# Performance work log

Measured on AMD Instinct MI355X. Metric: run time of the kernel, lower is better.

The kernel has to match this reference:

```python
import jax, jax.numpy as jnp
import numpy as np

B, T, D, H = 4096, 48, 64, 128
IMPUTE_WEIGHT = 0.3


def setup_inputs() -> dict:
    key = jax.random.key(0)
    ks = jax.random.split(key, 16)
    values = jax.random.normal(ks[0], (B, T, D), dtype=jnp.float32)
    masks = (jax.random.uniform(ks[1], (B, T, D)) < 0.7).astype(jnp.float32)
    deltas = jax.random.uniform(ks[2], (B, T, D), dtype=jnp.float32)
    s = 0.05
    return {
        "values": values, "masks": masks, "deltas": deltas,
        # TemporalDecay h (non-diag): Linear(D -> H)
        "W_td_h": jax.random.normal(ks[3], (H, D), dtype=jnp.float32) * s,
        "b_td_h": jax.random.normal(ks[4], (H,), dtype=jnp.float32) * s,
        # TemporalDecay x (diag): W is D x D but only diagonal used
        "W_td_x": jax.random.normal(ks[5], (D, D), dtype=jnp.float32) * s,
        "b_td_x": jax.random.normal(ks[6], (D,), dtype=jnp.float32) * s,
        # hist_reg: Linear(H -> D)
        "W_hist": jax.random.normal(ks[7], (D, H), dtype=jnp.float32) * s,
        "b_hist": jax.random.normal(ks[8], (D,), dtype=jnp.float32) * s,
        # feat_reg: D x D with zeroed diagonal mask
        "W_feat": jax.random.normal(ks[9], (D, D), dtype=jnp.float32) * s,
        "b_feat": jax.random.normal(ks[10], (D,), dtype=jnp.float32) * s,
        # weight_combine: Linear(2D -> D)
        "W_comb": jax.random.normal(ks[11], (D, 2 * D), dtype=jnp.float32) * s,
        "b_comb": jax.random.normal(ks[12], (D,), dtype=jnp.float32) * s,
        # LSTMCell(2D -> H), torch gate order i,f,g,o
        "W_ih": jax.random.normal(ks[13], (4 * H, 2 * D), dtype=jnp.float32) * s,
        "W_hh": jax.random.normal(ks[14], (4 * H, H), dtype=jnp.float32) * s,
        "b_ih": jnp.zeros((4 * H,), dtype=jnp.float32),
        "b_hh": jnp.zeros((4 * H,), dtype=jnp.float32),
    }


def reference(values, masks, deltas, W_td_h, b_td_h, W_td_x, b_td_x,
              W_hist, b_hist, W_feat, b_feat, W_comb, b_comb,
              W_ih, W_hh, b_ih, b_hh):
    Bn, Tn, Dn = values.shape
    Hn = W_hh.shape[1]
    w_td_x_diag = jnp.diagonal(W_td_x)                      # diag mask -> elementwise
    W_feat_m = W_feat * (1.0 - jnp.eye(Dn, dtype=W_feat.dtype))  # zero diagonal

    def step(carry, xs):
        h, c, x_loss = carry
        x, m, d = xs                                        # each [B, D]
        gamma_h = jnp.exp(-jax.nn.relu(d @ W_td_h.T + b_td_h))   # [B, H]
        gamma_x = jnp.exp(-jax.nn.relu(d * w_td_x_diag + b_td_x))  # [B, D]
        h = h * gamma_h
        x_h = h @ W_hist.T + b_hist
        denom = jnp.sum(m) + 1e-5
        x_loss = x_loss + jnp.sum(jnp.abs(x - x_h) * m) / denom
        x_c = m * x + (1.0 - m) * x_h
        z_h = x_c @ W_feat_m.T + b_feat
        x_loss = x_loss + jnp.sum(jnp.abs(x - z_h) * m) / denom
        alpha = jnp.concatenate([gamma_x, m], axis=1) @ W_comb.T + b_comb
        c_h = alpha * z_h + (1.0 - alpha) * x_h
        x_loss = x_loss + jnp.sum(jnp.abs(x - c_h) * m) / denom
        c_c = m * x + (1.0 - m) * c_h
        inp = jnp.concatenate([c_c, m], axis=1)             # [B, 2D]
        gates = inp @ W_ih.T + b_ih + h @ W_hh.T + b_hh     # [B, 4H]
        i_g, f_g, g_g, o_g = jnp.split(gates, 4, axis=1)
        c = jax.nn.sigmoid(f_g) * c + jax.nn.sigmoid(i_g) * jnp.tanh(g_g)
        h = jax.nn.sigmoid(o_g) * jnp.tanh(c)
        return (h, c, x_loss), c_c

    h0 = jnp.zeros((Bn, Hn), dtype=values.dtype)
    c0 = jnp.zeros((Bn, Hn), dtype=values.dtype)
    xs = (jnp.swapaxes(values, 0, 1), jnp.swapaxes(masks, 0, 1), jnp.swapaxes(deltas, 0, 1))
    (_, _, x_loss), imps = jax.lax.scan(step, (h0, c0, jnp.float32(0.0)), xs)
    imputations = jnp.swapaxes(imps, 0, 1)                  # [B, T, D]
    loss = x_loss * IMPUTE_WEIGHT
    return loss, imputations
```

## Files before the change

kernel.cpp:

```cpp
#include <hip/hip_runtime.h>
#include <cmath>

#define Bb 4096
#define Tt 48
#define Dd 64
#define Hh 128
#define NB 16
#define NTHR 512

typedef unsigned short ushort_t;
typedef __attribute__((ext_vector_type(8))) short short8;
typedef __attribute__((ext_vector_type(4))) float floatx4;

#define WS_DEN   0
#define WS_LOSS  48
#define WS_FRAGS 64
#define FR_F 0
#define FR_A 256
#define FR_B 272
#define FR_C 288
#define FR_E 296
#define N_FRAGS 312

__device__ __forceinline__ ushort_t f2bf(float x) {
  unsigned int u = __float_as_uint(x);
  u += 0x7fffu + ((u >> 16) & 1u);
  return (ushort_t)(u >> 16);
}
__device__ __forceinline__ float sigmoidf_(float x) { return 1.0f / (1.0f + __expf(-x)); }
__device__ __forceinline__ float tanhf_(float x) { return 2.0f / (1.0f + __expf(-2.0f * x)) - 1.0f; }

__global__ void prep_kernel(const float* __restrict__ W_td_h, const float* __restrict__ W_hist,
                            const float* __restrict__ W_feat, const float* __restrict__ W_comb,
                            const float* __restrict__ W_ih, const float* __restrict__ W_hh,
                            float* __restrict__ ws) {
  int f = blockIdx.x;
  int tid = threadIdx.x;
  if (f == 0 && tid < 64) ws[tid] = 0.0f;
  ushort_t* fb = (ushort_t*)(ws + WS_FRAGS);
  #pragma unroll
  for (int u = 0; u < 2; u++) {
    int e = tid * 2 + u;
    int l = e >> 3, j = e & 7;
    int n16 = l & 15;
    int kq = ((l >> 4) << 3) + j;
    float v;
    if (f < 256) {
      int w = f >> 5, g = (f >> 3) & 3, ks = f & 7;
      int n = g * 128 + w * 16 + n16;
      int k = ks * 32 + kq;
      v = (k < 128) ? W_ih[n * 128 + k] : W_hh[n * 128 + (k - 128)];
    } else if (f < 272) {
      int ff = f - 256, w = ff >> 1, ks = ff & 1;
      int n = w * 16 + n16;
      v = W_td_h[n * 64 + ks * 32 + kq];
    } else if (f < 288) {
      int ff = f - 272, w = ff >> 2, ks = ff & 3;
      int n = w * 16 + n16;
      v = W_hist[n * 128 + ks * 32 + kq];
    } else if (f < 296) {
      int ff = f - 288, w = ff >> 1, ks = ff & 1;
      int n = w * 16 + n16;
      int k = ks * 32 + kq;
      v = (n == k) ? 0.0f : W_feat[n * 64 + k];
    } else {
      int ff = f - 296, w = ff >> 2, ks = ff & 3;
      int n = w * 16 + n16;
      v = W_comb[n * 128 + ks * 32 + kq];
    }
    fb[f * 512 + e] = f2bf(v);
  }
}

__global__ void denom_kernel(const float* __restrict__ masks, float* __restrict__ ws) {
  int t = blockIdx.x >> 4;
  int chunk = blockIdx.x & 15;
  int base = chunk * 256;
  int tid = threadIdx.x;
  int j = tid & 63;
  int brow = tid >> 6;
  float s = 0.0f;
  for (int i = 0; i < 64; i++) {
    int b = base + i * 4 + brow;
    s += masks[((size_t)b * Tt + t) * Dd + j];
  }
  for (int off = 32; off > 0; off >>= 1) s += __shfl_down(s, off, 64);
  __shared__ float red[4];
  if ((tid & 63) == 0) red[tid >> 6] = s;
  __syncthreads();
  if (tid == 0) atomicAdd(&ws[WS_DEN + t], red[0] + red[1] + red[2] + red[3]);
}

__global__ __launch_bounds__(NTHR, 2)
void main_kernel(const float* __restrict__ values, const float* __restrict__ masks,
                 const float* __restrict__ deltas, const float* __restrict__ W_td_x,
                 const float* __restrict__ b_td_h, const float* __restrict__ b_td_x,
                 const float* __restrict__ b_hist, const float* __restrict__ b_feat,
                 const float* __restrict__ b_comb,
                 const float* __restrict__ b_ih, const float* __restrict__ b_hh,
                 float* ws, float* __restrict__ out) {
  __shared__ __align__(16) ushort_t act[16 * 264];
  __shared__ __align__(16) ushort_t dbuf[16 * 72];
  __shared__ __align__(16) ushort_t gxbuf[16 * 72];
  __shared__ __align__(16) ushort_t xcbuf[16 * 72];
  __shared__ __align__(16) float xmbuf[16 * 132];
  __shared__ __align__(16) float xhbuf[16 * 68];
  __shared__ float red[8];

  int tid = threadIdx.x;
  int w = tid >> 6;
  int lane = tid & 63;
  int l15 = lane & 15;
  int quad = lane >> 4;
  int b0 = blockIdx.x * NB;
  const ushort_t* fb = (const ushort_t*)(ws + WS_FRAGS);

  short8 wF[32];
  #pragma unroll
  for (int g = 0; g < 4; g++)
    #pragma unroll
    for (int ks = 0; ks < 8; ks++)
      wF[g * 8 + ks] = *(const short8*)(fb + (size_t)(FR_F + w * 32 + g * 8 + ks) * 512 + lane * 8);
  short8 wA[2];
  #pragma unroll
  for (int ks = 0; ks < 2; ks++)
    wA[ks] = *(const short8*)(fb + (size_t)(FR_A + w * 2 + ks) * 512 + lane * 8);
  short8 wBE[4];
  short8 wC[2];
  if (w < 4) {
    #pragma unroll
    for (int ks = 0; ks < 4; ks++)
      wBE[ks] = *(const short8*)(fb + (size_t)(FR_B + w * 4 + ks) * 512 + lane * 8);
  } else {
    #pragma unroll
    for (int ks = 0; ks < 4; ks++)
      wBE[ks] = *(const short8*)(fb + (size_t)(FR_E + (w - 4) * 4 + ks) * 512 + lane * 8);
    #pragma unroll
    for (int ks = 0; ks < 2; ks++)
      wC[ks] = *(const short8*)(fb + (size_t)(FR_C + (w - 4) * 2 + ks) * 512 + lane * 8);
  }

  int colh = w * 16 + l15;
  float biasF0 = b_ih[colh]       + b_hh[colh];
  float biasF1 = b_ih[128 + colh] + b_hh[128 + colh];
  float biasF2 = b_ih[256 + colh] + b_hh[256 + colh];
  float biasF3 = b_ih[384 + colh] + b_hh[384 + colh];
  float biasA  = b_td_h[colh];
  int colD = (w & 3) * 16 + l15;
  float biasBE = (w < 4) ? b_hist[colD] : b_comb[colD];
  float biasC  = b_feat[colD];

  int e0 = tid * 2;
  int lb = e0 >> 6, li = e0 & 63;
  size_t gbase = ((size_t)(b0 + lb) * Tt) * Dd + li;
  float diag0 = W_td_x[li * 64 + li], diag1 = W_td_x[(li + 1) * 64 + (li + 1)];
  float btx0 = b_td_x[li], btx1 = b_td_x[li + 1];

  int ha[4];
  float* impp[4];
  #pragma unroll
  for (int r = 0; r < 4; r++) {
    int m = quad * 4 + r;
    ha[r] = m * 264 + 128 + colh;
    impp[r] = out + 1 + (size_t)(b0 + m) * Tt * Dd + colD;
  }

  float h_reg[4] = {0.f, 0.f, 0.f, 0.f};
  float c_reg[4] = {0.f, 0.f, 0.f, 0.f};
  float loss_acc = 0.0f;

  float2 px = *(const float2*)(values + gbase);
  float2 pm = *(const float2*)(masks + gbase);
  float2 pd = *(const float2*)(deltas + gbase);

  for (int t = 0; t < Tt; t++) {
    __syncthreads();
    *(float4*)(&xmbuf[lb * 132 + 2 * li]) = make_float4(px.x, pm.x, px.y, pm.y);
    *(unsigned int*)(&act[lb * 264 + 64 + li]) =
        (unsigned int)f2bf(pm.x) | ((unsigned int)f2bf(pm.y) << 16);
    *(unsigned int*)(&dbuf[lb * 72 + li]) =
        (unsigned int)f2bf(pd.x) | ((unsigned int)f2bf(pd.y) << 16);
    float g0 = __expf(-fmaxf(pd.x * diag0 + btx0, 0.0f));
    float g1 = __expf(-fmaxf(pd.y * diag1 + btx1, 0.0f));
    *(unsigned int*)(&gxbuf[lb * 72 + li]) =
        (unsigned int)f2bf(g0) | ((unsigned int)f2bf(g1) << 16);
    float invden = 1.0f / (ws[WS_DEN + t] + 1e-5f);
    floatx4 a0 = {biasF0, biasF0, biasF0, biasF0};
    floatx4 a1 = {biasF1, biasF1, biasF1, biasF1};
    floatx4 a2 = {biasF2, biasF2, biasF2, biasF2};
    floatx4 a3 = {biasF3, biasF3, biasF3, biasF3};
    {
      int tn = (t + 1 < Tt) ? (t + 1) : t;
      size_t g = gbase + (size_t)tn * Dd;
      px = *(const float2*)(values + g);
      pm = *(const float2*)(masks + g);
      pd = *(const float2*)(deltas + g);
    }
    __syncthreads();

    short8 mf0 = *(const short8*)(&act[l15 * 264 + 64 + quad * 8]);
    short8 mf1 = *(const short8*)(&act[l15 * 264 + 96 + quad * 8]);
    {
      short8 df0 = *(const short8*)(&dbuf[l15 * 72 + quad * 8]);
      short8 df1 = *(const short8*)(&dbuf[l15 * 72 + 32 + quad * 8]);
      floatx4 accA = {biasA, biasA, biasA, biasA};
      accA = __builtin_amdgcn_mfma_f32_16x16x32_bf16(df0, wA[0], accA, 0, 0, 0);
      accA = __builtin_amdgcn_mfma_f32_16x16x32_bf16(df1, wA[1], accA, 0, 0, 0);
      a0 = __builtin_amdgcn_mfma_f32_16x16x32_bf16(mf0, wF[2],  a0, 0, 0, 0);
      a0 = __builtin_amdgcn_mfma_f32_16x16x32_bf16(mf1, wF[3],  a0, 0, 0, 0);
      a1 = __builtin_amdgcn_mfma_f32_16x16x32_bf16(mf0, wF[10], a1, 0, 0, 0);
      a1 = __builtin_amdgcn_mfma_f32_16x16x32_bf16(mf1, wF[11], a1, 0, 0, 0);
      a2 = __builtin_amdgcn_mfma_f32_16x16x32_bf16(mf0, wF[18], a2, 0, 0, 0);
      a2 = __builtin_amdgcn_mfma_f32_16x16x32_bf16(mf1, wF[19], a2, 0, 0, 0);
      a3 = __builtin_amdgcn_mfma_f32_16x16x32_bf16(mf0, wF[26], a3, 0, 0, 0);
      a3 = __builtin_amdgcn_mfma_f32_16x16x32_bf16(mf1, wF[27], a3, 0, 0, 0);
      #pragma unroll
      for (int r = 0; r < 4; r++) {
        h_reg[r] *= __expf(-fmaxf(accA[r], 0.0f));
        act[ha[r]] = f2bf(h_reg[r]);
      }
    }
    __syncthreads();

    floatx4 accP = {biasBE, biasBE, biasBE, biasBE};
    {
      short8 hf0 = *(const short8*)(&act[l15 * 264 + 128 + quad * 8]);
      short8 hf1 = *(const short8*)(&act[l15 * 264 + 160 + quad * 8]);
      short8 hf2 = *(const short8*)(&act[l15 * 264 + 192 + quad * 8]);
      short8 hf3 = *(const short8*)(&act[l15 * 264 + 224 + quad * 8]);
      if (w < 4) {
        accP = __builtin_amdgcn_mfma_f32_16x16x32_bf16(hf0, wBE[0], accP, 0, 0, 0);
        accP = __builtin_amdgcn_mfma_f32_16x16x32_bf16(hf1, wBE[1], accP, 0, 0, 0);
        accP = __builtin_amdgcn_mfma_f32_16x16x32_bf16(hf2, wBE[2], accP, 0, 0, 0);
        accP = __builtin_amdgcn_mfma_f32_16x16x32_bf16(hf3, wBE[3], accP, 0, 0, 0);
      } else {
        short8 gx0 = *(const short8*)(&gxbuf[l15 * 72 + quad * 8]);
        short8 gx1 = *(const short8*)(&gxbuf[l15 * 72 + 32 + quad * 8]);
        accP = __builtin_amdgcn_mfma_f32_16x16x32_bf16(gx0, wBE[0], accP, 0, 0, 0);
        accP = __builtin_amdgcn_mfma_f32_16x16x32_bf16(gx1, wBE[1], accP, 0, 0, 0);
        accP = __builtin_amdgcn_mfma_f32_16x16x32_bf16(mf0, wBE[2], accP, 0, 0, 0);
        accP = __builtin_amdgcn_mfma_f32_16x16x32_bf16(mf1, wBE[3], accP, 0, 0, 0);
      }
      a0 = __builtin_amdgcn_mfma_f32_16x16x32_bf16(hf0, wF[4],  a0, 0, 0, 0);
      a0 = __builtin_amdgcn_mfma_f32_16x16x32_bf16(hf1, wF[5],  a0, 0, 0, 0);
      a0 = __builtin_amdgcn_mfma_f32_16x16x32_bf16(hf2, wF[6],  a0, 0, 0, 0);
      a0 = __builtin_amdgcn_mfma_f32_16x16x32_bf16(hf3, wF[7],  a0, 0, 0, 0);
      a1 = __builtin_amdgcn_mfma_f32_16x16x32_bf16(hf0, wF[12], a1, 0, 0, 0);
      a1 = __builtin_amdgcn_mfma_f32_16x16x32_bf16(hf1, wF[13], a1, 0, 0, 0);
      a1 = __builtin_amdgcn_mfma_f32_16x16x32_bf16(hf2, wF[14], a1, 0, 0, 0);
      a1 = __builtin_amdgcn_mfma_f32_16x16x32_bf16(hf3, wF[15], a1, 0, 0, 0);
      a2 = __builtin_amdgcn_mfma_f32_16x16x32_bf16(hf0, wF[20], a2, 0, 0, 0);
      a2 = __builtin_amdgcn_mfma_f32_16x16x32_bf16(hf1, wF[21], a2, 0, 0, 0);
      a2 = __builtin_amdgcn_mfma_f32_16x16x32_bf16(hf2, wF[22], a2, 0, 0, 0);
      a2 = __builtin_amdgcn_mfma_f32_16x16x32_bf16(hf3, wF[23], a2, 0, 0, 0);
      a3 = __builtin_amdgcn_mfma_f32_16x16x32_bf16(hf0, wF[28], a3, 0, 0, 0);
      a3 = __builtin_amdgcn_mfma_f32_16x16x32_bf16(hf1, wF[29], a3, 0, 0, 0);
      a3 = __builtin_amdgcn_mfma_f32_16x16x32_bf16(hf2, wF[30], a3, 0, 0, 0);
      a3 = __builtin_amdgcn_mfma_f32_16x16x32_bf16(hf3, wF[31], a3, 0, 0, 0);
      if (w < 4) {
        #pragma unroll
        for (int r = 0; r < 4; r++) {
          int m = quad * 4 + r;
          float2 xm = *(const float2*)(&xmbuf[m * 132 + 2 * colD]);
          float xh = accP[r];
          loss_acc += fabsf(xm.x - xh) * xm.y * invden;
          xhbuf[m * 68 + colD] = xh;
          xcbuf[m * 72 + colD] = f2bf(xm.y * xm.x + (1.0f - xm.y) * xh);
        }
      }
    }
    __syncthreads();

    if (w >= 4) {
      short8 xc0 = *(const short8*)(&xcbuf[l15 * 72 + quad * 8]);
      short8 xc1 = *(const short8*)(&xcbuf[l15 * 72 + 32 + quad * 8]);
      floatx4 accC = {biasC, biasC, biasC, biasC};
      accC = __builtin_amdgcn_mfma_f32_16x16x32_bf16(xc0, wC[0], accC, 0, 0, 0);
      accC = __builtin_amdgcn_mfma_f32_16x16x32_bf16(xc1, wC[1], accC, 0, 0, 0);
      #pragma unroll
      for (int r = 0; r < 4; r++) {
        int m = quad * 4 + r;
        float2 xm = *(const float2*)(&xmbuf[m * 132 + 2 * colD]);
        float xh = xhbuf[m * 68 + colD];
        float zh = accC[r];
        float al = accP[r];
        loss_acc += fabsf(xm.x - zh) * xm.y * invden;
        float ch = al * zh + (1.0f - al) * xh;
        loss_acc += fabsf(xm.x - ch) * xm.y * invden;
        float cc = xm.y * xm.x + (1.0f - xm.y) * ch;
        *impp[r] = cc;
        impp[r] += Dd;
        act[m * 264 + colD] = f2bf(cc);
      }
    } else {
      #pragma unroll
      for (int r = 0; r < 4; r++) impp[r] += Dd;
    }
    __syncthreads();

    {
      short8 cf0 = *(const short8*)(&act[l15 * 264 + quad * 8]);
      short8 cf1 = *(const short8*)(&act[l15 * 264 + 32 + quad * 8]);
      a0 = __builtin_amdgcn_mfma_f32_16x16x32_bf16(cf0, wF[0],  a0, 0, 0, 0);
      a0 = __builtin_amdgcn_mfma_f32_16x16x32_bf16(cf1, wF[1],  a0, 0, 0, 0);
      a1 = __builtin_amdgcn_mfma_f32_16x16x32_bf16(cf0, wF[8],  a1, 0, 0, 0);
      a1 = __builtin_amdgcn_mfma_f32_16x16x32_bf16(cf1, wF[9],  a1, 0, 0, 0);
      a2 = __builtin_amdgcn_mfma_f32_16x16x32_bf16(cf0, wF[16], a2, 0, 0, 0);
      a2 = __builtin_amdgcn_mfma_f32_16x16x32_bf16(cf1, wF[17], a2, 0, 0, 0);
      a3 = __builtin_amdgcn_mfma_f32_16x16x32_bf16(cf0, wF[24], a3, 0, 0, 0);
      a3 = __builtin_amdgcn_mfma_f32_16x16x32_bf16(cf1, wF[25], a3, 0, 0, 0);
      #pragma unroll
      for (int r = 0; r < 4; r++) {
        float ig = sigmoidf_(a0[r]);
        float fg = sigmoidf_(a1[r]);
        float gg = tanhf_(a2[r]);
        float og = sigmoidf_(a3[r]);
        c_reg[r] = fg * c_reg[r] + ig * gg;
        h_reg[r] = og * tanhf_(c_reg[r]);
      }
    }
  }

  float s = loss_acc;
  for (int off = 32; off > 0; off >>= 1) s += __shfl_down(s, off, 64);
  if (lane == 0) red[w] = s;
  __syncthreads();
  if (tid == 0) {
    float tot = 0.0f;
    #pragma unroll
    for (int i = 0; i < 8; i++) tot += red[i];
    atomicAdd(&ws[WS_LOSS], tot);
  }
}

__global__ void final_kernel(const float* __restrict__ ws, float* __restrict__ out) {
  if (threadIdx.x == 0 && blockIdx.x == 0) out[0] = 0.3f * ws[WS_LOSS];
}

extern "C" void kernel_launch(void* const* d_in, const int* in_sizes, int n_in,
                              void* d_out, int out_size, void* d_ws, size_t ws_size,
                              hipStream_t stream) {
  const float* values = (const float*)d_in[0];
  const float* masks  = (const float*)d_in[1];
  const float* deltas = (const float*)d_in[2];
  const float* W_td_h = (const float*)d_in[3];
  const float* b_td_h = (const float*)d_in[4];
  const float* W_td_x = (const float*)d_in[5];
  const float* b_td_x = (const float*)d_in[6];
  const float* W_hist = (const float*)d_in[7];
  const float* b_hist = (const float*)d_in[8];
  const float* W_feat = (const float*)d_in[9];
  const float* b_feat = (const float*)d_in[10];
  const float* W_comb = (const float*)d_in[11];
  const float* b_comb = (const float*)d_in[12];
  const float* W_ih   = (const float*)d_in[13];
  const float* W_hh   = (const float*)d_in[14];
  const float* b_ih   = (const float*)d_in[15];
  const float* b_hh   = (const float*)d_in[16];
  float* out = (float*)d_out;
  float* ws  = (float*)d_ws;

  prep_kernel<<<dim3(N_FRAGS), dim3(256), 0, stream>>>(W_td_h, W_hist, W_feat, W_comb,
                                                       W_ih, W_hh, ws);
  denom_kernel<<<dim3(48 * 16), dim3(256), 0, stream>>>(masks, ws);
  main_kernel<<<dim3(Bb / NB), dim3(NTHR), 0, stream>>>(values, masks, deltas, W_td_x,
                                                        b_td_h, b_td_x, b_hist, b_feat,
                                                        b_comb, b_ih, b_hh, ws, out);
  final_kernel<<<dim3(1), dim3(64), 0, stream>>>(ws, out);
}
```

Baseline: 375.2 us.

## Split LSTM gate work across 16 waves and defer cell-update MFMAs

Doubles the block to 1024 threads so that each group of eight waves owns two of the four LSTM gates, and the workers for the hist, feat and comb regressions are spread over separate waves. Gate activations are exchanged through a new shared buffer. The c_c-dependent gate MFMAs and the cell update are deferred to the start of the next timestep, which removes one block barrier per step. The aim is more MFMA and VALU parallelism per CU and a shorter per-step dependency chain, at the cost of more shared memory, extra LDS traffic and tighter register limits under launch_bounds(1024,4).

```diff
diff --git a/kernel.cpp b/kernel.cpp
--- a/kernel.cpp
+++ b/kernel.cpp
@@ -6,7 +6,7 @@
 #define Dd 64
 #define Hh 128
 #define NB 16
-#define NTHR 512
+#define NTHR 1024
 
 typedef unsigned short ushort_t;
 typedef __attribute__((ext_vector_type(8))) short short8;
@@ -46,26 +46,26 @@
     int kq = ((l >> 4) << 3) + j;
     float v;
     if (f < 256) {
-      int w = f >> 5, g = (f >> 3) & 3, ks = f & 7;
-      int n = g * 128 + w * 16 + n16;
+      int cg = f >> 5, g = (f >> 3) & 3, ks = f & 7;
+      int n = g * 128 + cg * 16 + n16;
       int k = ks * 32 + kq;
       v = (k < 128) ? W_ih[n * 128 + k] : W_hh[n * 128 + (k - 128)];
     } else if (f < 272) {
-      int ff = f - 256, w = ff >> 1, ks = ff & 1;
-      int n = w * 16 + n16;
+      int ff = f - 256, cg = ff >> 1, ks = ff & 1;
+      int n = cg * 16 + n16;
       v = W_td_h[n * 64 + ks * 32 + kq];
     } else if (f < 288) {
-      int ff = f - 272, w = ff >> 2, ks = ff & 3;
-      int n = w * 16 + n16;
+      int ff = f - 272, cd = ff >> 2, ks = ff & 3;
+      int n = cd * 16 + n16;
       v = W_hist[n * 128 + ks * 32 + kq];
     } else if (f < 296) {
-      int ff = f - 288, w = ff >> 1, ks = ff & 1;
-      int n = w * 16 + n16;
+      int ff = f - 288, cd = ff >> 1, ks = ff & 1;
+      int n = cd * 16 + n16;
       int k = ks * 32 + kq;
       v = (n == k) ? 0.0f : W_feat[n * 64 + k];
     } else {
-      int ff = f - 296, w = ff >> 2, ks = ff & 3;
-      int n = w * 16 + n16;
+      int ff = f - 296, cd = ff >> 2, ks = ff & 3;
+      int n = cd * 16 + n16;
       v = W_comb[n * 128 + ks * 32 + kq];
     }
     fb[f * 512 + e] = f2bf(v);
@@ -91,7 +91,7 @@
   if (tid == 0) atomicAdd(&ws[WS_DEN + t], red[0] + red[1] + red[2] + red[3]);
 }
 
-__global__ __launch_bounds__(NTHR, 2)
+__global__ __launch_bounds__(NTHR, 4)
 void main_kernel(const float* __restrict__ values, const float* __restrict__ masks,
                  const float* __restrict__ deltas, const float* __restrict__ W_td_x,
                  const float* __restrict__ b_td_h, const float* __restrict__ b_td_x,
@@ -105,91 +105,108 @@
   __shared__ __align__(16) ushort_t xcbuf[16 * 72];
   __shared__ __align__(16) float xmbuf[16 * 132];
   __shared__ __align__(16) float xhbuf[16 * 68];
-  __shared__ float red[8];
+  __shared__ __align__(16) float pbuf[4096];
+  __shared__ float red[16];
 
   int tid = threadIdx.x;
   int w = tid >> 6;
   int lane = tid & 63;
   int l15 = lane & 15;
   int quad = lane >> 4;
+  int cg = w & 7;
+  bool lo = (w < 8);
   int b0 = blockIdx.x * NB;
   const ushort_t* fb = (const ushort_t*)(ws + WS_FRAGS);
 
-  short8 wF[32];
-  #pragma unroll
-  for (int g = 0; g < 4; g++)
-    #pragma unroll
-    for (int ks = 0; ks < 8; ks++)
-      wF[g * 8 + ks] = *(const short8*)(fb + (size_t)(FR_F + w * 32 + g * 8 + ks) * 512 + lane * 8);
-  short8 wA[2];
-  #pragma unroll
-  for (int ks = 0; ks < 2; ks++)
-    wA[ks] = *(const short8*)(fb + (size_t)(FR_A + w * 2 + ks) * 512 + lane * 8);
-  short8 wBE[4];
-  short8 wC[2];
-  if (w < 4) {
+  short8 wG[16];
+  {
+    int gb = lo ? 0 : 2;
+    #pragma unroll
+    for (int lg = 0; lg < 2; lg++)
+      #pragma unroll
+      for (int ks = 0; ks < 8; ks++)
+        wG[lg * 8 + ks] =
+            *(const short8*)(fb + (size_t)(FR_F + cg * 32 + (gb + lg) * 8 + ks) * 512 + lane * 8);
+  }
+  short8 wX[6];
+  if (lo) {
+    #pragma unroll
+    for (int ks = 0; ks < 2; ks++)
+      wX[ks] = *(const short8*)(fb + (size_t)(FR_A + cg * 2 + ks) * 512 + lane * 8);
+  } else if (w < 12) {
     #pragma unroll
     for (int ks = 0; ks < 4; ks++)
-      wBE[ks] = *(const short8*)(fb + (size_t)(FR_B + w * 4 + ks) * 512 + lane * 8);
+      wX[ks] = *(const short8*)(fb + (size_t)(FR_B + (w - 8) * 4 + ks) * 512 + lane * 8);
   } else {
     #pragma unroll
     for (int ks = 0; ks < 4; ks++)
-      wBE[ks] = *(const short8*)(fb + (size_t)(FR_E + (w - 4) * 4 + ks) * 512 + lane * 8);
+      wX[ks] = *(const short8*)(fb + (size_t)(FR_E + (w - 12) * 4 + ks) * 512 + lane * 8);
     #pragma unroll
     for (int ks = 0; ks < 2; ks++)
-      wC[ks] = *(const short8*)(fb + (size_t)(FR_C + (w - 4) * 2 + ks) * 512 + lane * 8);
-  }
-
-  int colh = w * 16 + l15;
-  float biasF0 = b_ih[colh]       + b_hh[colh];
-  float biasF1 = b_ih[128 + colh] + b_hh[128 + colh];
-  float biasF2 = b_ih[256 + colh] + b_hh[256 + colh];
-  float biasF3 = b_ih[384 + colh] + b_hh[384 + colh];
-  float biasA  = b_td_h[colh];
+      wX[4 + ks] = *(const short8*)(fb + (size_t)(FR_C + (w - 12) * 2 + ks) * 512 + lane * 8);
+  }
+
+  int colh = cg * 16 + l15;
+  float biasG0, biasG1;
+  if (lo) { biasG0 = b_ih[colh] + b_hh[colh];  biasG1 = b_ih[128 + colh] + b_hh[128 + colh]; }
+  else    { biasG0 = b_ih[256 + colh] + b_hh[256 + colh];  biasG1 = b_ih[384 + colh] + b_hh[384 + colh]; }
   int colD = (w & 3) * 16 + l15;
-  float biasBE = (w < 4) ? b_hist[colD] : b_comb[colD];
-  float biasC  = b_feat[colD];
+  float biasAC = lo ? b_td_h[colh] : b_feat[colD];
+  float biasBE = (w < 12) ? b_hist[colD] : b_comb[colD];
 
   int e0 = tid * 2;
   int lb = e0 >> 6, li = e0 & 63;
-  size_t gbase = ((size_t)(b0 + lb) * Tt) * Dd + li;
-  float diag0 = W_td_x[li * 64 + li], diag1 = W_td_x[(li + 1) * 64 + (li + 1)];
-  float btx0 = b_td_x[li], btx1 = b_td_x[li + 1];
-
-  int ha[4];
-  float* impp[4];
-  #pragma unroll
-  for (int r = 0; r < 4; r++) {
-    int m = quad * 4 + r;
-    ha[r] = m * 264 + 128 + colh;
-    impp[r] = out + 1 + (size_t)(b0 + m) * Tt * Dd + colD;
-  }
-
+  size_t gbase = 0;
+  float diag0 = 0, diag1 = 0, btx0 = 0, btx1 = 0;
+  float2 px, pm, pd;
+  if (lo) {
+    gbase = ((size_t)(b0 + lb) * Tt) * Dd + li;
+    diag0 = W_td_x[li * 64 + li];  diag1 = W_td_x[(li + 1) * 64 + (li + 1)];
+    btx0 = b_td_x[li];  btx1 = b_td_x[li + 1];
+    px = *(const float2*)(values + gbase);
+    pm = *(const float2*)(masks + gbase);
+    pd = *(const float2*)(deltas + gbase);
+  }
+
+  float* impt = out + 1;
+  if (w >= 12) impt = out + 1 + (size_t)(b0 + quad * 4) * (Tt * Dd) + colD;
+
+  floatx4 aG0, aG1, accP;
   float h_reg[4] = {0.f, 0.f, 0.f, 0.f};
   float c_reg[4] = {0.f, 0.f, 0.f, 0.f};
   float loss_acc = 0.0f;
 
-  float2 px = *(const float2*)(values + gbase);
-  float2 pm = *(const float2*)(masks + gbase);
-  float2 pd = *(const float2*)(deltas + gbase);
-
   for (int t = 0; t < Tt; t++) {
     __syncthreads();
-    *(float4*)(&xmbuf[lb * 132 + 2 * li]) = make_float4(px.x, pm.x, px.y, pm.y);
-    *(unsigned int*)(&act[lb * 264 + 64 + li]) =
-        (unsigned int)f2bf(pm.x) | ((unsigned int)f2bf(pm.y) << 16);
-    *(unsigned int*)(&dbuf[lb * 72 + li]) =
-        (unsigned int)f2bf(pd.x) | ((unsigned int)f2bf(pd.y) << 16);
-    float g0 = __expf(-fmaxf(pd.x * diag0 + btx0, 0.0f));
-    float g1 = __expf(-fmaxf(pd.y * diag1 + btx1, 0.0f));
-    *(unsigned int*)(&gxbuf[lb * 72 + li]) =
-        (unsigned int)f2bf(g0) | ((unsigned int)f2bf(g1) << 16);
+    if (t > 0) {
+      short8 cf0 = *(const short8*)(&act[l15 * 264 + quad * 8]);
+      short8 cf1 = *(const short8*)(&act[l15 * 264 + 32 + quad * 8]);
+      aG0 = __builtin_amdgcn_mfma_f32_16x16x32_bf16(cf0, wG[0], aG0, 0, 0, 0);
+      aG0 = __builtin_amdgcn_mfma_f32_16x16x32_bf16(cf1, wG[1], aG0, 0, 0, 0);
+      aG1 = __builtin_amdgcn_mfma_f32_16x16x32_bf16(cf0, wG[8], aG1, 0, 0, 0);
+      aG1 = __builtin_amdgcn_mfma_f32_16x16x32_bf16(cf1, wG[9], aG1, 0, 0, 0);
+      if (!lo) {
+        #pragma unroll
+        for (int r = 0; r < 4; r++) {
+          float tg = tanhf_(aG0[r]);
+          float so = sigmoidf_(aG1[r]);
+          *(float2*)(&pbuf[((r * 8 + cg) * 64 + lane) * 2]) = make_float2(tg, so);
+        }
+      }
+    }
+    if (lo) {
+      *(float4*)(&xmbuf[lb * 132 + 2 * li]) = make_float4(px.x, pm.x, px.y, pm.y);
+      *(unsigned int*)(&act[lb * 264 + 64 + li]) =
+          (unsigned int)f2bf(pm.x) | ((unsigned int)f2bf(pm.y) << 16);
+      *(unsigned int*)(&dbuf[lb * 72 + li]) =
+          (unsigned int)f2bf(pd.x) | ((unsigned int)f2bf(pd.y) << 16);
+      float g0 = __expf(-fmaxf(pd.x * diag0 + btx0, 0.0f));
+      float g1 = __expf(-fmaxf(pd.y * diag1 + btx1, 0.0f));
+      *(unsigned int*)(&gxbuf[lb * 72 + li]) =
+          (unsigned int)f2bf(g0) | ((unsigned int)f2bf(g1) << 16);
+    }
     float invden = 1.0f / (ws[WS_DEN + t] + 1e-5f);
-    floatx4 a0 = {biasF0, biasF0, biasF0, biasF0};
-    floatx4 a1 = {biasF1, biasF1, biasF1, biasF1};
-    floatx4 a2 = {biasF2, biasF2, biasF2, biasF2};
-    floatx4 a3 = {biasF3, biasF3, biasF3, biasF3};
-    {
+    if (lo) {
       int tn = (t + 1 < Tt) ? (t + 1) : t;
       size_t g = gbase + (size_t)tn * Dd;
       px = *(const float2*)(values + g);
@@ -198,71 +215,72 @@
     }
     __syncthreads();
 
-    short8 mf0 = *(const short8*)(&act[l15 * 264 + 64 + quad * 8]);
-    short8 mf1 = *(const short8*)(&act[l15 * 264 + 96 + quad * 8]);
-    {
-      short8 df0 = *(const short8*)(&dbuf[l15 * 72 + quad * 8]);
-      short8 df1 = *(const short8*)(&dbuf[l15 * 72 + 32 + quad * 8]);
-      floatx4 accA = {biasA, biasA, biasA, biasA};
-      accA = __builtin_amdgcn_mfma_f32_16x16x32_bf16(df0, wA[0], accA, 0, 0, 0);
-      accA = __builtin_amdgcn_mfma_f32_16x16x32_bf16(df1, wA[1], accA, 0, 0, 0);
-      a0 = __builtin_amdgcn_mfma_f32_16x16x32_bf16(mf0, wF[2],  a0, 0, 0, 0);
-      a0 = __builtin_amdgcn_mfma_f32_16x16x32_bf16(mf1, wF[3],  a0, 0, 0, 0);
-      a1 = __builtin_amdgcn_mfma_f32_16x16x32_bf16(mf0, wF[10], a1, 0, 0, 0);
-      a1 = __builtin_amdgcn_mfma_f32_16x16x32_bf16(mf1, wF[11], a1, 0, 0, 0);
-      a2 = __builtin_amdgcn_mfma_f32_16x16x32_bf16(mf0, wF[18], a2, 0, 0, 0);
-      a2 = __builtin_amdgcn_mfma_f32_16x16x32_bf16(mf1, wF[19], a2, 0, 0, 0);
-      a3 = __builtin_amdgcn_mfma_f32_16x16x32_bf16(mf0, wF[26], a3, 0, 0, 0);
-      a3 = __builtin_amdgcn_mfma_f32_16x16x32_bf16(mf1, wF[27], a3, 0, 0, 0);
+    if (lo && t > 0) {
       #pragma unroll
       for (int r = 0; r < 4; r++) {
-        h_reg[r] *= __expf(-fmaxf(accA[r], 0.0f));
-        act[ha[r]] = f2bf(h_reg[r]);
+        float2 p = *(const float2*)(&pbuf[((r * 8 + cg) * 64 + lane) * 2]);
+        float ig = sigmoidf_(aG0[r]);
+        float fg = sigmoidf_(aG1[r]);
+        c_reg[r] = fg * c_reg[r] + ig * p.x;
+        h_reg[r] = p.y * tanhf_(c_reg[r]);
+      }
+    }
+    aG0 = floatx4{biasG0, biasG0, biasG0, biasG0};
+    aG1 = floatx4{biasG1, biasG1, biasG1, biasG1};
+    {
+      short8 mf0 = *(const short8*)(&act[l15 * 264 + 64 + quad * 8]);
+      short8 mf1 = *(const short8*)(&act[l15 * 264 + 96 + quad * 8]);
+      aG0 = __builtin_amdgcn_mfma_f32_16x16x32_bf16(mf0, wG[2],  aG0, 0, 0, 0);
+      aG0 = __builtin_amdgcn_mfma_f32_16x16x32_bf16(mf1, wG[3],  aG0, 0, 0, 0);
+      aG1 = __builtin_amdgcn_mfma_f32_16x16x32_bf16(mf0, wG[10], aG1, 0, 0, 0);
+      aG1 = __builtin_amdgcn_mfma_f32_16x16x32_bf16(mf1, wG[11], aG1, 0, 0, 0);
+      if (lo) {
+        short8 df0 = *(const short8*)(&dbuf[l15 * 72 + quad * 8]);
+        short8 df1 = *(const short8*)(&dbuf[l15 * 72 + 32 + quad * 8]);
+        floatx4 accA = floatx4{biasAC, biasAC, biasAC, biasAC};
+        accA = __builtin_amdgcn_mfma_f32_16x16x32_bf16(df0, wX[0], accA, 0, 0, 0);
+        accA = __builtin_amdgcn_mfma_f32_16x16x32_bf16(df1, wX[1], accA, 0, 0, 0);
+        #pragma unroll
+        for (int r = 0; r < 4; r++) {
+          h_reg[r] *= __expf(-fmaxf(accA[r], 0.0f));
+          act[(quad * 4 + r) * 264 + 128 + colh] = f2bf(h_reg[r]);
+        }
+      } else if (w >= 12) {
+        short8 gx0 = *(const short8*)(&gxbuf[l15 * 72 + quad * 8]);
+        short8 gx1 = *(const short8*)(&gxbuf[l15 * 72 + 32 + quad * 8]);
+        accP = floatx4{biasBE, biasBE, biasBE, biasBE};
+        accP = __builtin_amdgcn_mfma_f32_16x16x32_bf16(gx0, wX[0], accP, 0, 0, 0);
+        accP = __builtin_amdgcn_mfma_f32_16x16x32_bf16(gx1, wX[1], accP, 0, 0, 0);
+        accP = __builtin_amdgcn_mfma_f32_16x16x32_bf16(mf0, wX[2], accP, 0, 0, 0);
+        accP = __builtin_amdgcn_mfma_f32_16x16x32_bf16(mf1, wX[3], accP, 0, 0, 0);
       }
     }
     __syncthreads();
 
-    floatx4 accP = {biasBE, biasBE, biasBE, biasBE};
     {
       short8 hf0 = *(const short8*)(&act[l15 * 264 + 128 + quad * 8]);
       short8 hf1 = *(const short8*)(&act[l15 * 264 + 160 + quad * 8]);
       short8 hf2 = *(const short8*)(&act[l15 * 264 + 192 + quad * 8]);
       short8 hf3 = *(const short8*)(&act[l15 * 264 + 224 + quad * 8]);
-      if (w < 4) {
-        accP = __builtin_amdgcn_mfma_f32_16x16x32_bf16(hf0, wBE[0], accP, 0, 0, 0);
-        accP = __builtin_amdgcn_mfma_f32_16x16x32_bf16(hf1, wBE[1], accP, 0, 0, 0);
-        accP = __builtin_amdgcn_mfma_f32_16x16x32_bf16(hf2, wBE[2], accP, 0, 0, 0);
-        accP = __builtin_amdgcn_mfma_f32_16x16x32_bf16(hf3, wBE[3], accP, 0, 0, 0);
-      } else {
-        short8 gx0 = *(const short8*)(&gxbuf[l15 * 72 + quad * 8]);
-        short8 gx1 = *(const short8*)(&gxbuf[l15 * 72 + 32 + quad * 8]);
-        accP = __builtin_amdgcn_mfma_f32_16x16x32_bf16(gx0, wBE[0], accP, 0, 0, 0);
-        accP = __builtin_amdgcn_mfma_f32_16x16x32_bf16(gx1, wBE[1], accP, 0, 0, 0);
-        accP = __builtin_amdgcn_mfma_f32_16x16x32_bf16(mf0, wBE[2], accP, 0, 0, 0);
-        accP = __builtin_amdgcn_mfma_f32_16x16x32_bf16(mf1, wBE[3], accP, 0, 0, 0);
-      }
-      a0 = __builtin_amdgcn_mfma_f32_16x16x32_bf16(hf0, wF[4],  a0, 0, 0, 0);
-      a0 = __builtin_amdgcn_mfma_f32_16x16x32_bf16(hf1, wF[5],  a0, 0, 0, 0);
-      a0 = __builtin_amdgcn_mfma_f32_16x16x32_bf16(hf2, wF[6],  a0, 0, 0, 0);
-      a0 = __builtin_amdgcn_mfma_f32_16x16x32_bf16(hf3, wF[7],  a0, 0, 0, 0);
-      a1 = __builtin_amdgcn_mfma_f32_16x16x32_bf16(hf0, wF[12], a1, 0, 0, 0);
-      a1 = __builtin_amdgcn_mfma_f32_16x16x32_bf16(hf1, wF[13], a1, 0, 0, 0);
-      a1 = __builtin_amdgcn_mfma_f32_16x16x32_bf16(hf2, wF[14], a1, 0, 0, 0);
-      a1 = __builtin_amdgcn_mfma_f32_16x16x32_bf16(hf3, wF[15], a1, 0, 0, 0);
-      a2 = __builtin_amdgcn_mfma_f32_16x16x32_bf16(hf0, wF[20], a2, 0, 0, 0);
-      a2 = __builtin_amdgcn_mfma_f32_16x16x32_bf16(hf1, wF[21], a2, 0, 0, 0);
-      a2 = __builtin_amdgcn_mfma_f32_16x16x32_bf16(hf2, wF[22], a2, 0, 0, 0);
-      a2 = __builtin_amdgcn_mfma_f32_16x16x32_bf16(hf3, wF[23], a2, 0, 0, 0);
-      a3 = __builtin_amdgcn_mfma_f32_16x16x32_bf16(hf0, wF[28], a3, 0, 0, 0);
-      a3 = __builtin_amdgcn_mfma_f32_16x16x32_bf16(hf1, wF[29], a3, 0, 0, 0);
-      a3 = __builtin_amdgcn_mfma_f32_16x16x32_bf16(hf2, wF[30], a3, 0, 0, 0);
-      a3 = __builtin_amdgcn_mfma_f32_16x16x32_bf16(hf3, wF[31], a3, 0, 0, 0);
-      if (w < 4) {
+      aG0 = __builtin_amdgcn_mfma_f32_16x16x32_bf16(hf0, wG[4],  aG0, 0, 0, 0);
+      aG0 = __builtin_amdgcn_mfma_f32_16x16x32_bf16(hf1, wG[5],  aG0, 0, 0, 0);
+      aG0 = __builtin_amdgcn_mfma_f32_16x16x32_bf16(hf2, wG[6],  aG0, 0, 0, 0);
+      aG0 = __builtin_amdgcn_mfma_f32_16x16x32_bf16(hf3, wG[7],  aG0, 0, 0, 0);
+      aG1 = __builtin_amdgcn_mfma_f32_16x16x32_bf16(hf0, wG[12], aG1, 0, 0, 0);
+      aG1 = __builtin_amdgcn_mfma_f32_16x16x32_bf16(hf1, wG[13], aG1, 0, 0, 0);
+      aG1 = __builtin_amdgcn_mfma_f32_16x16x32_bf16(hf2, wG[14], aG1, 0, 0, 0);
+      aG1 = __builtin_amdgcn_mfma_f32_16x16x32_bf16(hf3, wG[15], aG1, 0, 0, 0);
+      if (!lo && w < 12) {
+        floatx4 accB = floatx4{biasBE, biasBE, biasBE, biasBE};
+        accB = __builtin_amdgcn_mfma_f32_16x16x32_bf16(hf0, wX[0], accB, 0, 0, 0);
+        accB = __builtin_amdgcn_mfma_f32_16x16x32_bf16(hf1, wX[1], accB, 0, 0, 0);
+        accB = __builtin_amdgcn_mfma_f32_16x16x32_bf16(hf2, wX[2], accB, 0, 0, 0);
+        accB = __builtin_amdgcn_mfma_f32_16x16x32_bf16(hf3, wX[3], accB, 0, 0, 0);
         #pragma unroll
         for (int r = 0; r < 4; r++) {
           int m = quad * 4 + r;
           float2 xm = *(const float2*)(&xmbuf[m * 132 + 2 * colD]);
-          float xh = accP[r];
+          float xh = accB[r];
           loss_acc += fabsf(xm.x - xh) * xm.y * invden;
           xhbuf[m * 68 + colD] = xh;
           xcbuf[m * 72 + colD] = f2bf(xm.y * xm.x + (1.0f - xm.y) * xh);
@@ -271,53 +289,27 @@
     }
     __syncthreads();
 
-    if (w >= 4) {
+    if (w >= 12) {
       short8 xc0 = *(const short8*)(&xcbuf[l15 * 72 + quad * 8]);
       short8 xc1 = *(const short8*)(&xcbuf[l15 * 72 + 32 + quad * 8]);
-      floatx4 accC = {biasC, biasC, biasC, biasC};
-      accC = __builtin_amdgcn_mfma_f32_16x16x32_bf16(xc0, wC[0], accC, 0, 0, 0);
-      accC = __builtin_amdgcn_mfma_f32_16x16x32_bf16(xc1, wC[1], accC, 0, 0, 0);
+      floatx4 accC = floatx4{biasAC, biasAC, biasAC, biasAC};
+      accC = __builtin_amdgcn_mfma_f32_16x16x32_bf16(xc0, wX[4], accC, 0, 0, 0);
+      accC = __builtin_amdgcn_mfma_f32_16x16x32_bf16(xc1, wX[5], accC, 0, 0, 0);
       #pragma unroll
       for (int r = 0; r < 4; r++) {
         int m = quad * 4 + r;
         float2 xm = *(const float2*)(&xmbuf[m * 132 + 2 * colD]);
-        float xh = xhbuf[m * 68 + colD];
         float zh = accC[r];
         float al = accP[r];
+        float xh = xhbuf[m * 68 + colD];
         loss_acc += fabsf(xm.x - zh) * xm.y * invden;
         float ch = al * zh + (1.0f - al) * xh;
         loss_acc += fabsf(xm.x - ch) * xm.y * invden;
         float cc = xm.y * xm.x + (1.0f - xm.y) * ch;
-        *impp[r] = cc;
-        impp[r] += Dd;
+        impt[r * (Tt * Dd)] = cc;
         act[m * 264 + colD] = f2bf(cc);
       }
-    } else {
-      #pragma unroll
-      for (int r = 0; r < 4; r++) impp[r] += Dd;
-    }
-    __syncthreads();
-
-    {
-      short8 cf0 = *(const short8*)(&act[l15 * 264 + quad * 8]);
-      short8 cf1 = *(const short8*)(&act[l15 * 264 + 32 + quad * 8]);
-      a0 = __builtin_amdgcn_mfma_f32_16x16x32_bf16(cf0, wF[0],  a0, 0, 0, 0);
-      a0 = __builtin_amdgcn_mfma_f32_16x16x32_bf16(cf1, wF[1],  a0, 0, 0, 0);
-      a1 = __builtin_amdgcn_mfma_f32_16x16x32_bf16(cf0, wF[8],  a1, 0, 0, 0);
-      a1 = __builtin_amdgcn_mfma_f32_16x16x32_bf16(cf1, wF[9],  a1, 0, 0, 0);
-      a2 = __builtin_amdgcn_mfma_f32_16x16x32_bf16(cf0, wF[16], a2, 0, 0, 0);
-      a2 = __builtin_amdgcn_mfma_f32_16x16x32_bf16(cf1, wF[17], a2, 0, 0, 0);
-      a3 = __builtin_amdgcn_mfma_f32_16x16x32_bf16(cf0, wF[24], a3, 0, 0, 0);
-      a3 = __builtin_amdgcn_mfma_f32_16x16x32_bf16(cf1, wF[25], a3, 0, 0, 0);
-      #pragma unroll
-      for (int r = 0; r < 4; r++) {
-        float ig = sigmoidf_(a0[r]);
-        float fg = sigmoidf_(a1[r]);
-        float gg = tanhf_(a2[r]);
-        float og = sigmoidf_(a3[r]);
-        c_reg[r] = fg * c_reg[r] + ig * gg;
-        h_reg[r] = og * tanhf_(c_reg[r]);
-      }
+      impt += Dd;
     }
   }
 
@@ -328,7 +320,7 @@
   if (tid == 0) {
     float tot = 0.0f;
     #pragma unroll
-    for (int i = 0; i < 8; i++) tot += red[i];
+    for (int i = 0; i < 16; i++) tot += red[i];
     atomicAdd(&ws[WS_LOSS], tot);
   }
 }
```

After: 596.9 us. +59.1%, slower.
